# Optimization experiments

Measured on AMD Instinct MI355X. Metric: run time of the kernel, lower is better.

## Reference

```python
import jax, jax.numpy as jnp
import numpy as np

N_NODES = 100000
N_EDGES = 800000
D_MODEL = 128
N_HEAD = 8
LN_EPS = 1e-6


def setup_inputs() -> dict:
    key = jax.random.key(0)
    ks = jax.random.split(key, 6)
    embeds = jax.random.normal(ks[0], (N_NODES, D_MODEL), dtype=jnp.float32)
    # xavier_uniform bound for square [d, d] matrix: sqrt(6 / (d + d))
    bound = float(np.sqrt(6.0 / (D_MODEL + D_MODEL)))
    qW = jax.random.uniform(ks[1], (D_MODEL, D_MODEL), minval=-bound, maxval=bound, dtype=jnp.float32)
    kW = jax.random.uniform(ks[2], (D_MODEL, D_MODEL), minval=-bound, maxval=bound, dtype=jnp.float32)
    vW = jax.random.uniform(ks[3], (D_MODEL, D_MODEL), minval=-bound, maxval=bound, dtype=jnp.float32)
    ln_gamma = jnp.ones((D_MODEL,), dtype=jnp.float32)
    ln_beta = jnp.zeros((D_MODEL,), dtype=jnp.float32)
    edge_index = jax.random.randint(ks[4], (2, N_EDGES), 0, N_NODES, dtype=jnp.int64)
    return {"embeds": embeds, "qW": qW, "kW": kW, "vW": vW,
            "ln_gamma": ln_gamma, "ln_beta": ln_beta, "edge_index": edge_index}


def reference(embeds, qW, kW, vW, ln_gamma, ln_beta, edge_index):
    rows = edge_index[0]  # destination (softmax segment) indices, [E]
    cols = edge_index[1]  # source indices, [E]
    n_nodes, d_model = embeds.shape
    n_edges = rows.shape[0]
    head = N_HEAD
    d_head = d_model // head

    row_e = embeds[rows]                      # [E, d]
    col_e = embeds[cols]                      # [E, d]
    q = (row_e @ qW).reshape(n_edges, head, d_head)
    k = (col_e @ kW).reshape(n_edges, head, d_head)
    v = (col_e @ vW).reshape(n_edges, head, d_head)

    att = jnp.einsum('ehd,ehd->eh', q, k)     # [E, h]
    att = jnp.clip(att, -10.0, 10.0)
    exp_att = jnp.exp(att)

    # segment-softmax normalization over destination node
    att_norm = jax.ops.segment_sum(exp_att, rows, num_segments=n_nodes)  # [N, h]
    att = exp_att / (att_norm[rows] + 1e-8)   # [E, h]

    res_e = (att[:, :, None] * v).reshape(n_edges, d_model)              # [E, d]
    res = jax.ops.segment_sum(res_e, rows, num_segments=n_nodes)         # [N, d]
    res = res + embeds

    # LayerNorm(eps=1e-6) over last dim
    mean = jnp.mean(res, axis=-1, keepdims=True)
    var = jnp.mean((res - mean) ** 2, axis=-1, keepdims=True)
    out = (res - mean) * jax.lax.rsqrt(var + LN_EPS) * ln_gamma + ln_beta
    return out
```

## Files before the change

kernel.cpp:

```cpp
#include <hip/hip_runtime.h>
#include <hip/hip_bf16.h>

#define N_NODES 100000
#define N_EDGES 800000
#define D 128
#define NH 8
#define NB ((N_NODES + 255) / 256)
#define NBQ ((N_NODES + 63) / 64)

typedef __hip_bfloat16 bf16;
typedef __bf16 bf16x8 __attribute__((ext_vector_type(8)));
typedef float  f32x4  __attribute__((ext_vector_type(4)));

__device__ __forceinline__ unsigned short f2bu(float x) {
    bf16 b = __float2bfloat16(x);
    return *reinterpret_cast<unsigned short*>(&b);
}
__device__ __forceinline__ float bu2f(unsigned short u) {
    return __uint_as_float(((unsigned)u) << 16);
}
__device__ __forceinline__ float bfe0(unsigned u) { return __uint_as_float(u << 16); }
__device__ __forceinline__ float bfe1(unsigned u) { return __uint_as_float(u & 0xffff0000u); }

union frag_u { unsigned short u[8]; bf16x8 v; };

template<int CTRL>
__device__ __forceinline__ float dpp_add(float x) {
    int y = __builtin_amdgcn_mov_dpp(__float_as_int(x), CTRL, 0xf, 0xf, true);
    return x + __int_as_float(y);
}
__device__ __forceinline__ float red8(float x) {
    x = dpp_add<0xB1>(x);
    x = dpp_add<0x4E>(x);
    x = dpp_add<0x141>(x);
    return x;
}

__global__ __launch_bounds__(256) void prep_kernel(
    const float* __restrict__ Wq, const float* __restrict__ Wk, const float* __restrict__ Wv,
    unsigned short* __restrict__ Wf, int* __restrict__ counts)
{
    int t = blockIdx.x * 256 + threadIdx.x;
    if (t < N_NODES) counts[t] = 0;
    if (t < 3 * 32 * 64) {
        int lane = t & 63;
        int ct   = (t >> 6) & 31;
        int mat  = t >> 11;
        int c  = ct >> 3, tt = ct & 7;
        int n  = tt * 16 + (lane & 15);
        int kb = c * 32 + (lane >> 4) * 8;
        const float* W;
        int col;
        if (mat == 0) {
            W = Wq; col = n;
        } else {
            int g = (mat - 1) * 128 + n;
            W = (g & 2) ? Wv : Wk;
            col = ((g >> 2) << 1) | (g & 1);
        }
        unsigned short* dst = Wf + (size_t)mat * 32768 + (size_t)ct * 1024 + (size_t)lane * 8;
#pragma unroll
        for (int j = 0; j < 8; ++j) {
            float w  = W[(size_t)(kb + j) * D + col];
            unsigned short hb = f2bu(w);
            float lo = w - bu2f(hb);
            dst[j]       = hb;
            dst[512 + j] = f2bu(lo);
        }
    }
}

__global__ __launch_bounds__(256) void qkv_mfma(
    const float* __restrict__ E, const unsigned short* __restrict__ Wf,
    bf16* __restrict__ Q, char* __restrict__ KVb,
    const int* __restrict__ rows, int* __restrict__ counts)
{
    __shared__ unsigned short bsh[16384];
    const int tid  = threadIdx.x;
    const int wave = tid >> 6;
    const int lane = tid & 63;
    const int r0w  = blockIdx.x * 64 + wave * 16;

    {
        int e0 = (blockIdx.x * 256 + tid) * 2;
        if (e0 < N_EDGES) {
            int2 r2 = *reinterpret_cast<const int2*>(rows + e0);
            atomicAdd(&counts[r2.x], 1);
            atomicAdd(&counts[r2.y], 1);
        }
    }

    const int am = lane & 15;
    const int aq = lane >> 4;

    frag_u ahi[4], alo[4];
    {
        int row = r0w + am;
        if (row >= N_NODES) row = N_NODES - 1;
        const float* erow = E + (size_t)row * D + aq * 8;
#pragma unroll
        for (int c = 0; c < 4; ++c) {
            float4 e0 = *reinterpret_cast<const float4*>(erow + c * 32);
            float4 e1 = *reinterpret_cast<const float4*>(erow + c * 32 + 4);
            float ef[8] = {e0.x, e0.y, e0.z, e0.w, e1.x, e1.y, e1.z, e1.w};
#pragma unroll
            for (int j = 0; j < 8; ++j) {
                unsigned short hb = f2bu(ef[j]);
                ahi[c].u[j] = hb;
                alo[c].u[j] = f2bu(ef[j] - bu2f(hb));
            }
        }
    }

#pragma unroll
    for (int mat = 0; mat < 3; ++mat) {
        f32x4 acc[8];
#pragma unroll
        for (int t = 0; t < 8; ++t)
            acc[t] = (f32x4){0.f, 0.f, 0.f, 0.f};

        const unsigned short* wm = Wf + (size_t)mat * 32768;

#pragma unroll
        for (int half = 0; half < 2; ++half) {
            __syncthreads();
            const uint4* src = reinterpret_cast<const uint4*>(wm + half * 16384);
            uint4* dstv = reinterpret_cast<uint4*>(bsh);
#pragma unroll
            for (int k = 0; k < 8; ++k)
                dstv[k * 256 + tid] = src[k * 256 + tid];
            __syncthreads();

#pragma unroll
            for (int t = 0; t < 8; ++t) {
#pragma unroll
                for (int cc = 0; cc < 2; ++cc) {
                    const unsigned short* bp = bsh + (cc * 8 + t) * 1024 + lane * 8;
                    bf16x8 bhi = *reinterpret_cast<const bf16x8*>(bp);
                    bf16x8 blo = *reinterpret_cast<const bf16x8*>(bp + 512);
                    const int c = half * 2 + cc;
                    acc[t] = __builtin_amdgcn_mfma_f32_16x16x32_bf16(alo[c].v, bhi, acc[t], 0, 0, 0);
                    acc[t] = __builtin_amdgcn_mfma_f32_16x16x32_bf16(ahi[c].v, blo, acc[t], 0, 0, 0);
                    acc[t] = __builtin_amdgcn_mfma_f32_16x16x32_bf16(ahi[c].v, bhi, acc[t], 0, 0, 0);
                }
            }
        }
        __syncthreads();

        unsigned short* ob = bsh + wave * 2176;
#pragma unroll
        for (int t = 0; t < 8; ++t)
#pragma unroll
            for (int r = 0; r < 4; ++r)
                ob[(aq * 4 + r) * 136 + t * 16 + am] = f2bu(acc[t][r]);
        {
            const int row = lane >> 2, c4 = lane & 3;
            int grow = r0w + row;
            if (grow < N_NODES) {
                const uint4* srcb = reinterpret_cast<const uint4*>(ob + row * 136 + c4 * 32);
                uint4 d0 = srcb[0], d1 = srcb[1], d2 = srcb[2], d3 = srcb[3];
                uint4* dst;
                if (mat == 0)
                    dst = reinterpret_cast<uint4*>(Q + (size_t)grow * D + c4 * 32);
                else
                    dst = reinterpret_cast<uint4*>(KVb + ((size_t)grow << 9)
                                                   + (size_t)(mat - 1) * 256 + (size_t)c4 * 64);
                dst[0] = d0; dst[1] = d1; dst[2] = d2; dst[3] = d3;
            }
        }
    }
}

__global__ __launch_bounds__(256) void scan_block(
    const int* __restrict__ counts, int* __restrict__ scanned, int* __restrict__ block_sums)
{
    __shared__ int s[256];
    int tid = threadIdx.x;
    int i = blockIdx.x * 256 + tid;
    int v = (i < N_NODES) ? counts[i] : 0;
    s[tid] = v;
    __syncthreads();
#pragma unroll
    for (int off = 1; off < 256; off <<= 1) {
        int t = (tid >= off) ? s[tid - off] : 0;
        __syncthreads();
        s[tid] += t;
        __syncthreads();
    }
    if (i < N_NODES) scanned[i] = s[tid] - v;
    if (tid == 255) block_sums[blockIdx.x] = s[255];
}

__global__ __launch_bounds__(512) void scan_tops(int* __restrict__ block_sums)
{
    __shared__ int s[512];
    int tid = threadIdx.x;
    int v = (tid < NB) ? block_sums[tid] : 0;
    s[tid] = v;
    __syncthreads();
#pragma unroll
    for (int off = 1; off < 512; off <<= 1) {
        int t = (tid >= off) ? s[tid - off] : 0;
        __syncthreads();
        s[tid] += t;
        __syncthreads();
    }
    if (tid < NB) block_sums[tid] = s[tid] - v;
}

__global__ __launch_bounds__(256) void scan_add(
    int* __restrict__ scanned, const int* __restrict__ block_sums, int* __restrict__ cursor)
{
    int i = blockIdx.x * 256 + threadIdx.x;
    if (i < N_NODES) {
        int o = scanned[i] + block_sums[blockIdx.x];
        scanned[i] = o;
        cursor[i]  = o;
    }
}

__global__ __launch_bounds__(256) void scatter_kernel(
    const int* __restrict__ rows, const int* __restrict__ cols,
    int* __restrict__ cursor, int* __restrict__ csr_cols)
{
    int e = blockIdx.x * 256 + threadIdx.x;
    if (e < N_EDGES) {
        int pos = atomicAdd(&cursor[rows[e]], 1);
        csr_cols[pos] = cols[e];
    }
}

__device__ __forceinline__ void edge_body(
    const char* __restrict__ KVb, int off, unsigned lane8,
    float q0, float q1, float CLIP2,
    float& acc0, float& acc1, float& nrm)
{
    uint2 kv = *reinterpret_cast<const uint2*>(KVb + (unsigned)off + lane8);
    float p = q0 * bfe0(kv.x) + q1 * bfe1(kv.x);
    p = red8(p);
    float s = __builtin_amdgcn_exp2f(fminf(fmaxf(p, -CLIP2), CLIP2));
    nrm  += s;
    acc0 += s * bfe0(kv.y);
    acc1 += s * bfe1(kv.y);
}

__global__ __launch_bounds__(256) void fused_node(
    const bf16* __restrict__ Qb, const char* __restrict__ KVb,
    const int* __restrict__ offsets, const int* __restrict__ counts,
    const int* __restrict__ csr_cols,
    const float* __restrict__ emb,
    const float* __restrict__ gamma, const float* __restrict__ beta,
    float* __restrict__ out)
{
    int n = blockIdx.x * 4 + (threadIdx.x >> 6);
    int lane = threadIdx.x & 63;

    const float L2E   = 1.44269504f;
    const float CLIP2 = 14.4269504f;

    unsigned qu = *reinterpret_cast<const unsigned*>(Qb + (size_t)n * D + lane * 2);
    float q0 = bfe0(qu) * L2E, q1 = bfe1(qu) * L2E;

    int start = offsets[n];
    int cnt   = counts[n];
    unsigned lane8 = (unsigned)(lane << 3);

    float acc0a = 0.f, acc1a = 0.f, nrma = 0.f;
    float acc0b = 0.f, acc1b = 0.f, nrmb = 0.f;

    for (int base = 0; base < cnt; base += 64) {
        int m = cnt - base; if (m > 64) m = 64;
        int moff = (base + lane < cnt) ? (csr_cols[start + base + lane] << 9) : 0;
        int j = 0;
        for (; j + 7 < m; j += 8) {
            int o0 = __builtin_amdgcn_readlane(moff, j + 0);
            int o1 = __builtin_amdgcn_readlane(moff, j + 1);
            int o2 = __builtin_amdgcn_readlane(moff, j + 2);
            int o3 = __builtin_amdgcn_readlane(moff, j + 3);
            int o4 = __builtin_amdgcn_readlane(moff, j + 4);
            int o5 = __builtin_amdgcn_readlane(moff, j + 5);
            int o6 = __builtin_amdgcn_readlane(moff, j + 6);
            int o7 = __builtin_amdgcn_readlane(moff, j + 7);
            edge_body(KVb, o0, lane8, q0, q1, CLIP2, acc0a, acc1a, nrma);
            edge_body(KVb, o1, lane8, q0, q1, CLIP2, acc0b, acc1b, nrmb);
            edge_body(KVb, o2, lane8, q0, q1, CLIP2, acc0a, acc1a, nrma);
            edge_body(KVb, o3, lane8, q0, q1, CLIP2, acc0b, acc1b, nrmb);
            edge_body(KVb, o4, lane8, q0, q1, CLIP2, acc0a, acc1a, nrma);
            edge_body(KVb, o5, lane8, q0, q1, CLIP2, acc0b, acc1b, nrmb);
            edge_body(KVb, o6, lane8, q0, q1, CLIP2, acc0a, acc1a, nrma);
            edge_body(KVb, o7, lane8, q0, q1, CLIP2, acc0b, acc1b, nrmb);
        }
        for (; j + 3 < m; j += 4) {
            int o0 = __builtin_amdgcn_readlane(moff, j + 0);
            int o1 = __builtin_amdgcn_readlane(moff, j + 1);
            int o2 = __builtin_amdgcn_readlane(moff, j + 2);
            int o3 = __builtin_amdgcn_readlane(moff, j + 3);
            edge_body(KVb, o0, lane8, q0, q1, CLIP2, acc0a, acc1a, nrma);
            edge_body(KVb, o1, lane8, q0, q1, CLIP2, acc0b, acc1b, nrmb);
            edge_body(KVb, o2, lane8, q0, q1, CLIP2, acc0a, acc1a, nrma);
            edge_body(KVb, o3, lane8, q0, q1, CLIP2, acc0b, acc1b, nrmb);
        }
        for (; j < m; ++j) {
            int o0 = __builtin_amdgcn_readlane(moff, j);
            edge_body(KVb, o0, lane8, q0, q1, CLIP2, acc0a, acc1a, nrma);
        }
    }

    float nrm  = nrma + nrmb;
    float acc0 = acc0a + acc0b;
    float acc1 = acc1a + acc1b;

    float w = 1.f / (nrm + 1e-8f);
    float2 e2 = *reinterpret_cast<const float2*>(emb + (size_t)n * D + lane * 2);
    float x0 = acc0 * w + e2.x;
    float x1 = acc1 * w + e2.y;

    float s1 = x0 + x1;
    float s2 = x0 * x0 + x1 * x1;
#pragma unroll
    for (int off = 32; off; off >>= 1) {
        s1 += __shfl_xor(s1, off, 64);
        s2 += __shfl_xor(s2, off, 64);
    }
    float mean = s1 * (1.0f / 128.0f);
    float var  = fmaxf(s2 * (1.0f / 128.0f) - mean * mean, 0.f);
    float rs = rsqrtf(var + 1e-6f);

    float d0 = x0 - mean, d1 = x1 - mean;
    float2 g2 = *reinterpret_cast<const float2*>(gamma + lane * 2);
    float2 b2 = *reinterpret_cast<const float2*>(beta + lane * 2);
    float2 o2 = make_float2(d0 * rs * g2.x + b2.x, d1 * rs * g2.y + b2.y);
    *reinterpret_cast<float2*>(out + (size_t)n * D + lane * 2) = o2;
}

extern "C" void kernel_launch(void* const* d_in, const int* in_sizes, int n_in,
                              void* d_out, int out_size, void* d_ws, size_t ws_size,
                              hipStream_t stream)
{
    const float* emb   = (const float*)d_in[0];
    const float* qW    = (const float*)d_in[1];
    const float* kW    = (const float*)d_in[2];
    const float* vW    = (const float*)d_in[3];
    const float* gamma = (const float*)d_in[4];
    const float* beta  = (const float*)d_in[5];
    const int*   eidx  = (const int*)d_in[6];
    const int*   rows  = eidx;
    const int*   cols  = eidx + N_EDGES;
    float* out = (float*)d_out;

    const size_t ND = (size_t)N_NODES * D;
    bf16* Qb  = (bf16*)d_ws;
    char* KVb = (char*)(Qb + ND);
    int* counts     = (int*)(KVb + (size_t)N_NODES * 512);
    int* offsets    = counts + N_NODES;
    int* cursor     = offsets + N_NODES;
    int* block_sums = cursor + N_NODES;
    int* csr_cols   = block_sums + 512;
    unsigned short* Wf = (unsigned short*)(csr_cols + N_EDGES);

    prep_kernel<<<NB, 256, 0, stream>>>(qW, kW, vW, Wf, counts);
    qkv_mfma<<<NBQ, 256, 0, stream>>>(emb, Wf, Qb, KVb, rows, counts);

    scan_block<<<NB, 256, 0, stream>>>(counts, offsets, block_sums);
    scan_tops<<<1, 512, 0, stream>>>(block_sums);
    scan_add<<<NB, 256, 0, stream>>>(offsets, block_sums, cursor);
    scatter_kernel<<<(N_EDGES + 255) / 256, 256, 0, stream>>>(rows, cols, cursor, csr_cols);

    fused_node<<<(N_NODES + 3) / 4, 256, 0, stream>>>(
        Qb, KVb, offsets, counts, csr_cols, emb, gamma, beta, out);
}
```

Baseline: 283.8 us.

## Fuse CSR build into single cooperative kernel with grid syncs

Replaces the separate count, three-stage scan and scatter kernels with one cooperative kernel that zeroes counts, histograms rows, runs a wave-level scan with an atomic global ticket for chunk bases, and scatters columns, separated by grid.sync. Edge counting is removed from the QKV projection kernel. This cuts kernel launches and inter-kernel gaps, but the ticket-based offsets are not ordered by node and the histogram no longer overlaps with the matmul. Grid syncs add their own latency.

Result: slower. 575.7 us (+102.9%).

```diff
diff --git a/kernel.cpp b/kernel.cpp
--- a/kernel.cpp
+++ b/kernel.cpp
@@ -1,12 +1,15 @@
 #include <hip/hip_runtime.h>
 #include <hip/hip_bf16.h>
+#include <hip/hip_cooperative_groups.h>
+
+namespace cg = cooperative_groups;
 
 #define N_NODES 100000
 #define N_EDGES 800000
 #define D 128
 #define NH 8
-#define NB ((N_NODES + 255) / 256)
 #define NBQ ((N_NODES + 63) / 64)
+#define COOP_BLOCKS 1024
 
 typedef __hip_bfloat16 bf16;
 typedef __bf16 bf16x8 __attribute__((ext_vector_type(8)));
@@ -38,57 +41,95 @@
 
 __global__ __launch_bounds__(256) void prep_kernel(
     const float* __restrict__ Wq, const float* __restrict__ Wk, const float* __restrict__ Wv,
-    unsigned short* __restrict__ Wf, int* __restrict__ counts)
+    unsigned short* __restrict__ Wf)
 {
     int t = blockIdx.x * 256 + threadIdx.x;
-    if (t < N_NODES) counts[t] = 0;
-    if (t < 3 * 32 * 64) {
-        int lane = t & 63;
-        int ct   = (t >> 6) & 31;
-        int mat  = t >> 11;
-        int c  = ct >> 3, tt = ct & 7;
-        int n  = tt * 16 + (lane & 15);
-        int kb = c * 32 + (lane >> 4) * 8;
-        const float* W;
-        int col;
-        if (mat == 0) {
-            W = Wq; col = n;
-        } else {
-            int g = (mat - 1) * 128 + n;
-            W = (g & 2) ? Wv : Wk;
-            col = ((g >> 2) << 1) | (g & 1);
-        }
-        unsigned short* dst = Wf + (size_t)mat * 32768 + (size_t)ct * 1024 + (size_t)lane * 8;
-#pragma unroll
-        for (int j = 0; j < 8; ++j) {
-            float w  = W[(size_t)(kb + j) * D + col];
-            unsigned short hb = f2bu(w);
-            float lo = w - bu2f(hb);
-            dst[j]       = hb;
-            dst[512 + j] = f2bu(lo);
-        }
+    if (t >= 3 * 32 * 64) return;
+    int lane = t & 63;
+    int ct   = (t >> 6) & 31;
+    int mat  = t >> 11;
+    int c  = ct >> 3, tt = ct & 7;
+    int n  = tt * 16 + (lane & 15);
+    int kb = c * 32 + (lane >> 4) * 8;
+    const float* W;
+    int col;
+    if (mat == 0) {
+        W = Wq; col = n;
+    } else {
+        int g = (mat - 1) * 128 + n;
+        W = (g & 2) ? Wv : Wk;
+        col = ((g >> 2) << 1) | (g & 1);
+    }
+    unsigned short* dst = Wf + (size_t)mat * 32768 + (size_t)ct * 1024 + (size_t)lane * 8;
+#pragma unroll
+    for (int j = 0; j < 8; ++j) {
+        float w  = W[(size_t)(kb + j) * D + col];
+        unsigned short hb = f2bu(w);
+        float lo = w - bu2f(hb);
+        dst[j]       = hb;
+        dst[512 + j] = f2bu(lo);
+    }
+}
+
+__global__ __launch_bounds__(256) void csr_coop(
+    const int* __restrict__ rows, const int* __restrict__ cols,
+    int* __restrict__ counts, int* __restrict__ offsets,
+    int* __restrict__ cursor, int* __restrict__ csr_cols,
+    int* __restrict__ gcur)
+{
+    cg::grid_group grid = cg::this_grid();
+    const int tid  = blockIdx.x * 256 + threadIdx.x;
+    const int nthr = gridDim.x * 256;
+
+    for (int i = tid; i < N_NODES; i += nthr) counts[i] = 0;
+    if (tid == 0) *gcur = 0;
+    grid.sync();
+
+    for (int e = tid; e < N_EDGES; e += nthr)
+        atomicAdd(&counts[rows[e]], 1);
+    grid.sync();
+
+    {
+        const int wid  = tid >> 6, lane = tid & 63;
+        const int nwav = nthr >> 6;
+        const int nchunk = (N_NODES + 63) / 64;
+        for (int c = wid; c < nchunk; c += nwav) {
+            int n = c * 64 + lane;
+            int v = (n < N_NODES) ? counts[n] : 0;
+            int s = v;
+#pragma unroll
+            for (int d = 1; d < 64; d <<= 1) {
+                int t = __shfl_up(s, d, 64);
+                if (lane >= d) s += t;
+            }
+            int tot = __shfl(s, 63, 64);
+            int base = 0;
+            if (lane == 0) base = atomicAdd(gcur, tot);
+            base = __shfl(base, 0, 64);
+            if (n < N_NODES) {
+                int o = base + s - v;
+                offsets[n] = o;
+                cursor[n]  = o;
+            }
+        }
+    }
+    grid.sync();
+
+    for (int e = tid; e < N_EDGES; e += nthr) {
+        int pos = atomicAdd(&cursor[rows[e]], 1);
+        csr_cols[pos] = cols[e];
     }
 }
 
 __global__ __launch_bounds__(256) void qkv_mfma(
     const float* __restrict__ E, const unsigned short* __restrict__ Wf,
-    bf16* __restrict__ Q, char* __restrict__ KVb,
-    const int* __restrict__ rows, int* __restrict__ counts)
+    bf16* __restrict__ Q, char* __restrict__ KVb)
 {
     __shared__ unsigned short bsh[16384];
     const int tid  = threadIdx.x;
     const int wave = tid >> 6;
     const int lane = tid & 63;
     const int r0w  = blockIdx.x * 64 + wave * 16;
-
-    {
-        int e0 = (blockIdx.x * 256 + tid) * 2;
-        if (e0 < N_EDGES) {
-            int2 r2 = *reinterpret_cast<const int2*>(rows + e0);
-            atomicAdd(&counts[r2.x], 1);
-            atomicAdd(&counts[r2.y], 1);
-        }
-    }
 
     const int am = lane & 15;
     const int aq = lane >> 4;
@@ -168,65 +209,6 @@
                 dst[0] = d0; dst[1] = d1; dst[2] = d2; dst[3] = d3;
             }
         }
-    }
-}
-
-__global__ __launch_bounds__(256) void scan_block(
-    const int* __restrict__ counts, int* __restrict__ scanned, int* __restrict__ block_sums)
-{
-    __shared__ int s[256];
-    int tid = threadIdx.x;
-    int i = blockIdx.x * 256 + tid;
-    int v = (i < N_NODES) ? counts[i] : 0;
-    s[tid] = v;
-    __syncthreads();
-#pragma unroll
-    for (int off = 1; off < 256; off <<= 1) {
-        int t = (tid >= off) ? s[tid - off] : 0;
-        __syncthreads();
-        s[tid] += t;
-        __syncthreads();
-    }
-    if (i < N_NODES) scanned[i] = s[tid] - v;
-    if (tid == 255) block_sums[blockIdx.x] = s[255];
-}
-
-__global__ __launch_bounds__(512) void scan_tops(int* __restrict__ block_sums)
-{
-    __shared__ int s[512];
-    int tid = threadIdx.x;
-    int v = (tid < NB) ? block_sums[tid] : 0;
-    s[tid] = v;
-    __syncthreads();
-#pragma unroll
-    for (int off = 1; off < 512; off <<= 1) {
-        int t = (tid >= off) ? s[tid - off] : 0;
-        __syncthreads();
-        s[tid] += t;
-        __syncthreads();
-    }
-    if (tid < NB) block_sums[tid] = s[tid] - v;
-}
-
-__global__ __launch_bounds__(256) void scan_add(
-    int* __restrict__ scanned, const int* __restrict__ block_sums, int* __restrict__ cursor)
-{
-    int i = blockIdx.x * 256 + threadIdx.x;
-    if (i < N_NODES) {
-        int o = scanned[i] + block_sums[blockIdx.x];
-        scanned[i] = o;
-        cursor[i]  = o;
-    }
-}
-
-__global__ __launch_bounds__(256) void scatter_kernel(
-    const int* __restrict__ rows, const int* __restrict__ cols,
-    int* __restrict__ cursor, int* __restrict__ csr_cols)
-{
-    int e = blockIdx.x * 256 + threadIdx.x;
-    if (e < N_EDGES) {
-        int pos = atomicAdd(&cursor[rows[e]], 1);
-        csr_cols[pos] = cols[e];
     }
 }
 
@@ -354,17 +336,20 @@
     int* counts     = (int*)(KVb + (size_t)N_NODES * 512);
     int* offsets    = counts + N_NODES;
     int* cursor     = offsets + N_NODES;
-    int* block_sums = cursor + N_NODES;
-    int* csr_cols   = block_sums + 512;
+    int* csr_cols   = cursor + N_NODES;
     unsigned short* Wf = (unsigned short*)(csr_cols + N_EDGES);
-
-    prep_kernel<<<NB, 256, 0, stream>>>(qW, kW, vW, Wf, counts);
-    qkv_mfma<<<NBQ, 256, 0, stream>>>(emb, Wf, Qb, KVb, rows, counts);
-
-    scan_block<<<NB, 256, 0, stream>>>(counts, offsets, block_sums);
-    scan_tops<<<1, 512, 0, stream>>>(block_sums);
-    scan_add<<<NB, 256, 0, stream>>>(offsets, block_sums, cursor);
-    scatter_kernel<<<(N_EDGES + 255) / 256, 256, 0, stream>>>(rows, cols, cursor, csr_cols);
+    int* gcur       = (int*)(Wf + 3 * 32768);
+
+    prep_kernel<<<24, 256, 0, stream>>>(qW, kW, vW, Wf);
+
+    {
+        void* args[] = {(void*)&rows, (void*)&cols, (void*)&counts, (void*)&offsets,
+                        (void*)&cursor, (void*)&csr_cols, (void*)&gcur};
+        hipLaunchCooperativeKernel((const void*)csr_coop, dim3(COOP_BLOCKS), dim3(256),
+                                   args, 0, stream);
+    }
+
+    qkv_mfma<<<NBQ, 256, 0, stream>>>(emb, Wf, Qb, KVb);
 
     fused_node<<<(N_NODES + 3) / 4, 256, 0, stream>>>(
         Qb, KVb, offsets, counts, csr_cols, emb, gamma, beta, out);
```
